# Performance work log

Hardware: AMD Instinct MI355X
Metric: run time of the kernel (lower is better)

Reference implementation:

```python
import jax, jax.numpy as jnp
import numpy as np

N = 500_000          # num nodes
K = 3                # neighbors per star subgraph = graphlet_size - 1
E = N * K            # one subgraph per node -> directed (center, nbr) edges
L = 2                # hop_neighbor
FD = 2               # final_dim = 2**pqc_dim
H = 64               # hidden_dim
NC = 8               # num_classes
NIN = 16             # node_input_dim
EIN = 8              # edge_input_dim


def _lin(k, i, o):
    # torch.nn.Linear-style init scale
    return jax.random.normal(k, (i, o), jnp.float32) * (1.0 / np.sqrt(i))


def setup_inputs() -> dict:
    key = jax.random.key(0)
    ks = jax.random.split(key, 32)
    node_feat = jax.random.normal(ks[0], (N, NIN), jnp.float32)
    edge_attr = jax.random.normal(ks[1], (E, EIN), jnp.float32)
    # edge e = (center, neighbor); centers grouped: edges 3i..3i+2 belong to node i
    centers = jnp.repeat(jnp.arange(N, dtype=jnp.int32), K)
    neighbors = jax.random.randint(ks[2], (E,), 0, N, dtype=jnp.int32)
    edge_index = jnp.stack([centers, neighbors])  # [2, E]
    batch = jnp.zeros((N,), jnp.int32)
    msg_W1 = jnp.stack([_lin(ks[6 + i], 2 * FD, H) for i in range(L)])
    msg_W2 = jnp.stack([_lin(ks[8 + i], H, FD) for i in range(L)])
    upd_W1 = jnp.stack([_lin(ks[10 + i], 2 * FD, H) for i in range(L)])
    upd_W2 = jnp.stack([_lin(ks[12 + i], H, FD) for i in range(L)])
    return dict(
        node_feat=node_feat, edge_attr=edge_attr, edge_index=edge_index, batch=batch,
        Wn=_lin(ks[3], NIN, FD), bn=jnp.zeros((FD,), jnp.float32),
        We=_lin(ks[4], EIN, FD), be=jnp.zeros((FD,), jnp.float32),
        msg_W1=msg_W1, msg_b1=jnp.zeros((L, H), jnp.float32),
        msg_W2=msg_W2, msg_b2=jnp.zeros((L, FD), jnp.float32),
        upd_W1=upd_W1, upd_b1=jnp.zeros((L, H), jnp.float32),
        upd_W2=upd_W2, upd_b2=jnp.zeros((L, FD), jnp.float32),
        fin_W1=_lin(ks[14], FD, H), fin_b1=jnp.zeros((H,), jnp.float32),
        fin_W2=_lin(ks[15], H, NC), fin_b2=jnp.zeros((NC,), jnp.float32),
    )


def _leaky(x):
    return jnp.where(x >= 0, x, 0.1 * x)


def _mlp(x, W1, b1, W2, b2):
    # MLP([din, 64, dout], act=LeakyReLU(0.1)); dropout inactive at eval
    return _leaky(x @ W1 + b1) @ W2 + b2


def reference(node_feat, edge_attr, edge_index, batch, Wn, bn, We, be,
              msg_W1, msg_b1, msg_W2, msg_b2, upd_W1, upd_b1, upd_W2, upd_b2,
              fin_W1, fin_b1, fin_W2, fin_b2):
    ctr = edge_index[0]  # [E] center of each star edge
    nbr = edge_index[1]  # [E] neighbor
    h = node_feat @ Wn + bn      # [N, FD] input_node projection
    e = edge_attr @ We + be      # [E, FD] input_edge projection (fixed across layers)
    for l in range(L):
        # message over each (center, neighbor) edge: concat(edge_feat, nbr_feat)
        msg = _mlp(jnp.concatenate([e, h[nbr]], axis=1),
                   msg_W1[l], msg_b1[l], msg_W2[l], msg_b2[l])  # [E, FD]
        aggr = jax.ops.segment_sum(msg, ctr, num_segments=N)    # [N, FD]
        new = _mlp(jnp.concatenate([h, aggr], axis=1),
                   upd_W1[l], upd_b1[l], upd_W2[l], upd_b2[l])  # [N, FD]
        h = jax.nn.relu(h + new)  # updates_node[center] += new_center; then ReLU
    return _mlp(h, fin_W1, fin_b1, fin_W2, fin_b2)  # [N, NC]
```

## Files before the change

kernel.cpp:

```cpp
#include <hip/hip_runtime.h>

#define NN 500000
#define KK 3
#define EE (NN * KK)
#define HH 64
#define NC 8
#define NIN 16
#define EIN 8

typedef __attribute__((ext_vector_type(2)))  float sf2;
typedef __attribute__((ext_vector_type(4)))  float sf4;
typedef __attribute__((ext_vector_type(8)))  float sf8;
typedef __attribute__((ext_vector_type(16))) float sf16;

__device__ __forceinline__ sf2 sload2(const float* p) {
    sf2 r; asm("s_load_dwordx2 %0, %1, 0x0" : "=s"(r) : "s"(p)); return r;
}
__device__ __forceinline__ sf4 sload4(const float* p) {
    sf4 r; asm("s_load_dwordx4 %0, %1, 0x0" : "=s"(r) : "s"(p)); return r;
}
__device__ __forceinline__ sf8 sload8(const float* p) {
    sf8 r; asm("s_load_dwordx8 %0, %1, 0x0" : "=s"(r) : "s"(p)); return r;
}
__device__ __forceinline__ sf16 sload16(const float* p) {
    sf16 r; asm("s_load_dwordx16 %0, %1, 0x0" : "=s"(r) : "s"(p)); return r;
}

#define SWAIT1(a)           asm volatile("s_waitcnt lgkmcnt(0)" : "+s"(a))
#define SWAIT2(a,b)         asm volatile("s_waitcnt lgkmcnt(0)" : "+s"(a),"+s"(b))
#define SWAIT5(a,b,c,d,e)   asm volatile("s_waitcnt lgkmcnt(0)" : "+s"(a),"+s"(b),"+s"(c),"+s"(d),"+s"(e))
#define SWAIT6(a,b,c,d,e,f) asm volatile("s_waitcnt lgkmcnt(0)" : "+s"(a),"+s"(b),"+s"(c),"+s"(d),"+s"(e),"+s"(f))

__device__ __forceinline__ float leaky(float x) { return fmaxf(x, 0.1f * x); }

__global__ __launch_bounds__(256) void prep_kernel(
    const float* __restrict__ node_feat, const float* __restrict__ edge_attr,
    const float* __restrict__ Wn, const float* __restrict__ bn,
    const float* __restrict__ We, const float* __restrict__ be,
    float* __restrict__ h, float* __restrict__ ep)
{
    sf16 wn0 = sload16(Wn);
    sf16 wn1 = sload16(Wn + 16);
    sf2  bnv = sload2(bn);
    sf16 wev = sload16(We);
    sf2  bev = sload2(be);
    SWAIT5(wn0, wn1, bnv, wev, bev);

    int idx = blockIdx.x * 256 + threadIdx.x;
    if (idx < NN) {
        const float4* x4 = (const float4*)(node_feat + (size_t)idx * NIN);
        float4 v0 = x4[0], v1 = x4[1], v2 = x4[2], v3 = x4[3];
        float xs[16] = {v0.x, v0.y, v0.z, v0.w, v1.x, v1.y, v1.z, v1.w,
                        v2.x, v2.y, v2.z, v2.w, v3.x, v3.y, v3.z, v3.w};
        float a0 = bnv.x, a1 = bnv.y;
#pragma unroll
        for (int i = 0; i < 8; i++) {
            a0 = fmaf(xs[i], wn0[2 * i], a0);
            a1 = fmaf(xs[i], wn0[2 * i + 1], a1);
        }
#pragma unroll
        for (int i = 0; i < 8; i++) {
            a0 = fmaf(xs[8 + i], wn1[2 * i], a0);
            a1 = fmaf(xs[8 + i], wn1[2 * i + 1], a1);
        }
        ((float2*)h)[idx] = make_float2(a0, a1);
    } else if (idx < NN + EE) {
        int eidx = idx - NN;
        const float4* x4 = (const float4*)(edge_attr + (size_t)eidx * EIN);
        float4 v0 = x4[0], v1 = x4[1];
        float xs[8] = {v0.x, v0.y, v0.z, v0.w, v1.x, v1.y, v1.z, v1.w};
        float a0 = bev.x, a1 = bev.y;
#pragma unroll
        for (int i = 0; i < 8; i++) {
            a0 = fmaf(xs[i], wev[2 * i], a0);
            a1 = fmaf(xs[i], wev[2 * i + 1], a1);
        }
        ((float2*)ep)[eidx] = make_float2(a0, a1);
    }
}

template<bool FINAL>
__global__ __launch_bounds__(256) void layer_kernel(
    const float* __restrict__ h_in, const float* __restrict__ e,
    const int* __restrict__ nbr,
    const float* __restrict__ mW1, const float* __restrict__ mb1,
    const float* __restrict__ mW2, const float* __restrict__ mb2,
    const float* __restrict__ uW1, const float* __restrict__ ub1,
    const float* __restrict__ uW2, const float* __restrict__ ub2,
    float* __restrict__ h_out,
    const float* __restrict__ fW1, const float* __restrict__ fb1,
    const float* __restrict__ fW2, const float* __restrict__ fb2,
    float* __restrict__ out)
{
    int i = blockIdx.x * 256 + threadIdx.x;
    if (i >= NN) return;

    sf2 mb2v = sload2(mb2);
    sf2 ub2v = sload2(ub2);
    SWAIT2(mb2v, ub2v);

    float2 hh = ((const float2*)h_in)[i];
    int base = i * KK;
    int n0 = nbr[base + 0], n1 = nbr[base + 1], n2 = nbr[base + 2];
    float2 hn0 = ((const float2*)h_in)[n0];
    float2 hn1 = ((const float2*)h_in)[n1];
    float2 hn2 = ((const float2*)h_in)[n2];
    float2 e0 = ((const float2*)e)[base + 0];
    float2 e1 = ((const float2*)e)[base + 1];
    float2 e2 = ((const float2*)e)[base + 2];

    float a0 = 3.0f * mb2v.x, a1 = 3.0f * mb2v.y;
#pragma unroll 1
    for (int j0 = 0; j0 < HH; j0 += 8) {
        sf8 w0 = sload8(mW1 + j0);
        sf8 w1 = sload8(mW1 + HH + j0);
        sf8 w2 = sload8(mW1 + 2 * HH + j0);
        sf8 w3 = sload8(mW1 + 3 * HH + j0);
        sf8 bb = sload8(mb1 + j0);
        sf16 wc = sload16(mW2 + 2 * j0);
        SWAIT6(w0, w1, w2, w3, bb, wc);
#pragma unroll
        for (int q = 0; q < 8; q++) {
            float t0 = fmaf(e0.x, w0[q], fmaf(e0.y, w1[q], fmaf(hn0.x, w2[q], fmaf(hn0.y, w3[q], bb[q]))));
            float t1 = fmaf(e1.x, w0[q], fmaf(e1.y, w1[q], fmaf(hn1.x, w2[q], fmaf(hn1.y, w3[q], bb[q]))));
            float t2 = fmaf(e2.x, w0[q], fmaf(e2.y, w1[q], fmaf(hn2.x, w2[q], fmaf(hn2.y, w3[q], bb[q]))));
            float ts = leaky(t0) + leaky(t1) + leaky(t2);
            a0 = fmaf(ts, wc[2 * q], a0);
            a1 = fmaf(ts, wc[2 * q + 1], a1);
        }
    }

    float u0 = ub2v.x, u1 = ub2v.y;
#pragma unroll 1
    for (int j0 = 0; j0 < HH; j0 += 8) {
        sf8 w0 = sload8(uW1 + j0);
        sf8 w1 = sload8(uW1 + HH + j0);
        sf8 w2 = sload8(uW1 + 2 * HH + j0);
        sf8 w3 = sload8(uW1 + 3 * HH + j0);
        sf8 bb = sload8(ub1 + j0);
        sf16 wc = sload16(uW2 + 2 * j0);
        SWAIT6(w0, w1, w2, w3, bb, wc);
#pragma unroll
        for (int q = 0; q < 8; q++) {
            float tt = fmaf(hh.x, w0[q], fmaf(hh.y, w1[q], fmaf(a0, w2[q], fmaf(a1, w3[q], bb[q]))));
            tt = leaky(tt);
            u0 = fmaf(tt, wc[2 * q], u0);
            u1 = fmaf(tt, wc[2 * q + 1], u1);
        }
    }
    float nh0 = fmaxf(hh.x + u0, 0.0f);
    float nh1 = fmaxf(hh.y + u1, 0.0f);

    if (!FINAL) {
        ((float2*)h_out)[i] = make_float2(nh0, nh1);
    } else {
        sf8 fb2v = sload8(fb2);
        SWAIT1(fb2v);
        float o[NC];
#pragma unroll
        for (int c = 0; c < NC; c++) o[c] = fb2v[c];
#pragma unroll 1
        for (int j0 = 0; j0 < HH; j0 += 4) {
            sf4 p0 = sload4(fW1 + j0);
            sf4 p1 = sload4(fW1 + HH + j0);
            sf4 pb = sload4(fb1 + j0);
            sf16 q0 = sload16(fW2 + 8 * j0);
            sf16 q1 = sload16(fW2 + 8 * j0 + 16);
            SWAIT5(p0, p1, pb, q0, q1);
#pragma unroll
            for (int qq = 0; qq < 4; qq++) {
                float tt = leaky(fmaf(nh0, p0[qq], fmaf(nh1, p1[qq], pb[qq])));
#pragma unroll
                for (int c = 0; c < NC; c++) {
                    float wv = (qq < 2) ? q0[8 * qq + c] : q1[8 * (qq - 2) + c];
                    o[c] = fmaf(tt, wv, o[c]);
                }
            }
        }
        float4* op = (float4*)(out + (size_t)i * NC);
        op[0] = make_float4(o[0], o[1], o[2], o[3]);
        op[1] = make_float4(o[4], o[5], o[6], o[7]);
    }
}

extern "C" void kernel_launch(void* const* d_in, const int* in_sizes, int n_in,
                              void* d_out, int out_size, void* d_ws, size_t ws_size,
                              hipStream_t stream) {
    const float* node_feat = (const float*)d_in[0];
    const float* edge_attr = (const float*)d_in[1];
    const int* edge_index = (const int*)d_in[2];
    const float* Wn = (const float*)d_in[4];
    const float* bn = (const float*)d_in[5];
    const float* We = (const float*)d_in[6];
    const float* be = (const float*)d_in[7];
    const float* msgW1 = (const float*)d_in[8];
    const float* msgb1 = (const float*)d_in[9];
    const float* msgW2 = (const float*)d_in[10];
    const float* msgb2 = (const float*)d_in[11];
    const float* updW1 = (const float*)d_in[12];
    const float* updb1 = (const float*)d_in[13];
    const float* updW2 = (const float*)d_in[14];
    const float* updb2 = (const float*)d_in[15];
    const float* finW1 = (const float*)d_in[16];
    const float* finb1 = (const float*)d_in[17];
    const float* finW2 = (const float*)d_in[18];
    const float* finb2 = (const float*)d_in[19];
    float* out = (float*)d_out;

    const int* nbr = edge_index + EE;

    char* ws = (char*)d_ws;
    float* hA = (float*)ws;
    float* hB = (float*)(ws + (size_t)NN * 2 * 4);
    float* eP = (float*)(ws + (size_t)NN * 4 * 4);

    const int threads = 256;
    int prep_grid = (NN + EE + threads - 1) / threads;
    prep_kernel<<<prep_grid, threads, 0, stream>>>(node_feat, edge_attr, Wn, bn, We, be, hA, eP);

    int grid = (NN + threads - 1) / threads;
    layer_kernel<false><<<grid, threads, 0, stream>>>(
        hA, eP, nbr,
        msgW1, msgb1, msgW2, msgb2,
        updW1, updb1, updW2, updb2,
        hB, finW1, finb1, finW2, finb2, nullptr);
    layer_kernel<true><<<grid, threads, 0, stream>>>(
        hB, eP, nbr,
        msgW1 + 4 * HH, msgb1 + HH, msgW2 + 2 * HH, msgb2 + 2,
        updW1 + 4 * HH, updb1 + HH, updW2 + 2 * HH, updb2 + 2,
        nullptr, finW1, finb1, finW2, finb2, out);
}
```

Baseline: 213.9 us.

## Compute MLP hidden layers in packed fp16 with pre-packed weights and fdot2

Adds a pack kernel that converts the message, update and final MLP weights into interleaved fp16 pairs. The layer kernels then evaluate the hidden units two at a time with packed fp16 FMA, apply leaky ReLU in packed form, and reduce with fdot2 into fp32 accumulators. Edge projections are stored as duplicated fp16 pairs. The aim is to halve the VALU instruction count of the compute-bound per-node MLPs, at the cost of fp16 rounding error in the hidden activations and one extra small launch.

```diff
diff --git a/kernel.cpp b/kernel.cpp
--- a/kernel.cpp
+++ b/kernel.cpp
@@ -8,36 +8,100 @@
 #define NIN 16
 #define EIN 8
 
+typedef __attribute__((ext_vector_type(2))) _Float16 h2;
 typedef __attribute__((ext_vector_type(2)))  float sf2;
-typedef __attribute__((ext_vector_type(4)))  float sf4;
 typedef __attribute__((ext_vector_type(8)))  float sf8;
 typedef __attribute__((ext_vector_type(16))) float sf16;
 
+using pk_t = decltype(__builtin_amdgcn_cvt_pkrtz(0.f, 0.f));
+
 __device__ __forceinline__ sf2 sload2(const float* p) {
     sf2 r; asm("s_load_dwordx2 %0, %1, 0x0" : "=s"(r) : "s"(p)); return r;
 }
-__device__ __forceinline__ sf4 sload4(const float* p) {
-    sf4 r; asm("s_load_dwordx4 %0, %1, 0x0" : "=s"(r) : "s"(p)); return r;
-}
 __device__ __forceinline__ sf8 sload8(const float* p) {
     sf8 r; asm("s_load_dwordx8 %0, %1, 0x0" : "=s"(r) : "s"(p)); return r;
 }
 __device__ __forceinline__ sf16 sload16(const float* p) {
     sf16 r; asm("s_load_dwordx16 %0, %1, 0x0" : "=s"(r) : "s"(p)); return r;
 }
-
-#define SWAIT1(a)           asm volatile("s_waitcnt lgkmcnt(0)" : "+s"(a))
-#define SWAIT2(a,b)         asm volatile("s_waitcnt lgkmcnt(0)" : "+s"(a),"+s"(b))
-#define SWAIT5(a,b,c,d,e)   asm volatile("s_waitcnt lgkmcnt(0)" : "+s"(a),"+s"(b),"+s"(c),"+s"(d),"+s"(e))
-#define SWAIT6(a,b,c,d,e,f) asm volatile("s_waitcnt lgkmcnt(0)" : "+s"(a),"+s"(b),"+s"(c),"+s"(d),"+s"(e),"+s"(f))
-
-__device__ __forceinline__ float leaky(float x) { return fmaxf(x, 0.1f * x); }
+#define SWAIT1(a)       asm volatile("s_waitcnt lgkmcnt(0)" : "+s"(a))
+#define SWAIT2(a,b)     asm volatile("s_waitcnt lgkmcnt(0)" : "+s"(a),"+s"(b))
+#define SWAIT3(a,b,c)   asm volatile("s_waitcnt lgkmcnt(0)" : "+s"(a),"+s"(b),"+s"(c))
+#define SWAIT5(a,b,c,d,e) asm volatile("s_waitcnt lgkmcnt(0)" : "+s"(a),"+s"(b),"+s"(c),"+s"(d),"+s"(e))
+
+#if __has_builtin(__builtin_elementwise_fma)
+#define PKFMA(a,b,c) __builtin_elementwise_fma((a),(b),(c))
+#else
+#define PKFMA(a,b,c) ((a)*(b)+(c))
+#endif
+
+__device__ __forceinline__ h2 bch2(float f)        { return __builtin_bit_cast(h2, f); }
+__device__ __forceinline__ h2 bch2u(unsigned int u){ return __builtin_bit_cast(h2, u); }
+__device__ __forceinline__ h2 dup16(float f) {
+    return __builtin_bit_cast(h2, __builtin_amdgcn_cvt_pkrtz(f, f));
+}
+__device__ __forceinline__ float fdot2(h2 a, h2 b, float c) {
+#if __has_builtin(__builtin_amdgcn_fdot2)
+    return __builtin_amdgcn_fdot2(__builtin_bit_cast(pk_t, a),
+                                  __builtin_bit_cast(pk_t, b), c, false);
+#else
+    return c + (float)a.x * (float)b.x + (float)a.y * (float)b.y;
+#endif
+}
+__device__ __forceinline__ h2 lk2(h2 x) {
+    h2 c = {(_Float16)0.1f, (_Float16)0.1f};
+    return __builtin_elementwise_max(x, x * c);
+}
+
+__device__ __forceinline__ float pack2(float a, float b) {
+    h2 v; v.x = (_Float16)a; v.y = (_Float16)b;
+    return __builtin_bit_cast(float, v);
+}
+
+__global__ void pack_kernel(
+    const float* __restrict__ msgW1, const float* __restrict__ msgb1, const float* __restrict__ msgW2,
+    const float* __restrict__ updW1, const float* __restrict__ updb1, const float* __restrict__ updW2,
+    const float* __restrict__ finW1, const float* __restrict__ finb1, const float* __restrict__ finW2,
+    float* __restrict__ wpack)
+{
+    int t = threadIdx.x;
+    if (t < 32) {
+        int l = t >> 4, which = (t >> 3) & 1, c = t & 7;
+        const float* W1 = (which ? updW1 : msgW1) + l * 4 * HH;
+        const float* b1 = (which ? updb1 : msgb1) + l * HH;
+        const float* W2 = (which ? updW2 : msgW2) + l * 2 * HH;
+        float* dst = wpack + (l * 2 + which) * 256 + c * 32;
+        int j0 = c * 8;
+        for (int r = 0; r < 4; r++)
+            for (int p = 0; p < 4; p++)
+                dst[r * 4 + p] = pack2(W1[r * HH + j0 + 2 * p], W1[r * HH + j0 + 2 * p + 1]);
+        for (int p = 0; p < 4; p++) {
+            dst[16 + p] = pack2(b1[j0 + 2 * p], b1[j0 + 2 * p + 1]);
+            dst[20 + p] = pack2(W2[(j0 + 2 * p) * 2 + 0], W2[(j0 + 2 * p + 1) * 2 + 0]);
+            dst[24 + p] = pack2(W2[(j0 + 2 * p) * 2 + 1], W2[(j0 + 2 * p + 1) * 2 + 1]);
+            dst[28 + p] = 0.0f;
+        }
+    } else if (t < 40) {
+        int c = t - 32, j0 = c * 8;
+        float* dst = wpack + 1024 + c * 48;
+        for (int p = 0; p < 4; p++) {
+            dst[p]      = pack2(finW1[j0 + 2 * p],      finW1[j0 + 2 * p + 1]);
+            dst[4 + p]  = pack2(finW1[HH + j0 + 2 * p], finW1[HH + j0 + 2 * p + 1]);
+            dst[8 + p]  = pack2(finb1[j0 + 2 * p],      finb1[j0 + 2 * p + 1]);
+            dst[12 + p] = 0.0f;
+        }
+        for (int jp = 0; jp < 4; jp++)
+            for (int cc = 0; cc < NC; cc++)
+                dst[16 + jp * 8 + cc] = pack2(finW2[(j0 + 2 * jp) * NC + cc],
+                                              finW2[(j0 + 2 * jp + 1) * NC + cc]);
+    }
+}
 
 __global__ __launch_bounds__(256) void prep_kernel(
     const float* __restrict__ node_feat, const float* __restrict__ edge_attr,
     const float* __restrict__ Wn, const float* __restrict__ bn,
     const float* __restrict__ We, const float* __restrict__ be,
-    float* __restrict__ h, float* __restrict__ ep)
+    float* __restrict__ h, unsigned int* __restrict__ ep)
 {
     sf16 wn0 = sload16(Wn);
     sf16 wn1 = sload16(Wn + 16);
@@ -75,21 +139,21 @@
             a0 = fmaf(xs[i], wev[2 * i], a0);
             a1 = fmaf(xs[i], wev[2 * i + 1], a1);
         }
-        ((float2*)ep)[eidx] = make_float2(a0, a1);
+        uint2 pe;
+        pe.x = __builtin_bit_cast(unsigned int, dup16(a0));
+        pe.y = __builtin_bit_cast(unsigned int, dup16(a1));
+        ((uint2*)ep)[eidx] = pe;
     }
 }
 
 template<bool FINAL>
 __global__ __launch_bounds__(256) void layer_kernel(
-    const float* __restrict__ h_in, const float* __restrict__ e,
+    const float* __restrict__ h_in, const unsigned int* __restrict__ eP,
     const int* __restrict__ nbr,
-    const float* __restrict__ mW1, const float* __restrict__ mb1,
-    const float* __restrict__ mW2, const float* __restrict__ mb2,
-    const float* __restrict__ uW1, const float* __restrict__ ub1,
-    const float* __restrict__ uW2, const float* __restrict__ ub2,
+    const float* __restrict__ mblk, const float* __restrict__ mb2,
+    const float* __restrict__ ublk, const float* __restrict__ ub2,
     float* __restrict__ h_out,
-    const float* __restrict__ fW1, const float* __restrict__ fb1,
-    const float* __restrict__ fW2, const float* __restrict__ fb2,
+    const float* __restrict__ fblk, const float* __restrict__ fb2,
     float* __restrict__ out)
 {
     int i = blockIdx.x * 256 + threadIdx.x;
@@ -102,50 +166,55 @@
     float2 hh = ((const float2*)h_in)[i];
     int base = i * KK;
     int n0 = nbr[base + 0], n1 = nbr[base + 1], n2 = nbr[base + 2];
-    float2 hn0 = ((const float2*)h_in)[n0];
-    float2 hn1 = ((const float2*)h_in)[n1];
-    float2 hn2 = ((const float2*)h_in)[n2];
-    float2 e0 = ((const float2*)e)[base + 0];
-    float2 e1 = ((const float2*)e)[base + 1];
-    float2 e2 = ((const float2*)e)[base + 2];
+    float2 g0 = ((const float2*)h_in)[n0];
+    float2 g1 = ((const float2*)h_in)[n1];
+    float2 g2 = ((const float2*)h_in)[n2];
+    uint2 pe0 = ((const uint2*)eP)[base + 0];
+    uint2 pe1 = ((const uint2*)eP)[base + 1];
+    uint2 pe2 = ((const uint2*)eP)[base + 2];
+    h2 e0x = bch2u(pe0.x), e0y = bch2u(pe0.y);
+    h2 e1x = bch2u(pe1.x), e1y = bch2u(pe1.y);
+    h2 e2x = bch2u(pe2.x), e2y = bch2u(pe2.y);
+    h2 n0x = dup16(g0.x), n0y = dup16(g0.y);
+    h2 n1x = dup16(g1.x), n1y = dup16(g1.y);
+    h2 n2x = dup16(g2.x), n2y = dup16(g2.y);
 
     float a0 = 3.0f * mb2v.x, a1 = 3.0f * mb2v.y;
 #pragma unroll 1
-    for (int j0 = 0; j0 < HH; j0 += 8) {
-        sf8 w0 = sload8(mW1 + j0);
-        sf8 w1 = sload8(mW1 + HH + j0);
-        sf8 w2 = sload8(mW1 + 2 * HH + j0);
-        sf8 w3 = sload8(mW1 + 3 * HH + j0);
-        sf8 bb = sload8(mb1 + j0);
-        sf16 wc = sload16(mW2 + 2 * j0);
-        SWAIT6(w0, w1, w2, w3, bb, wc);
-#pragma unroll
-        for (int q = 0; q < 8; q++) {
-            float t0 = fmaf(e0.x, w0[q], fmaf(e0.y, w1[q], fmaf(hn0.x, w2[q], fmaf(hn0.y, w3[q], bb[q]))));
-            float t1 = fmaf(e1.x, w0[q], fmaf(e1.y, w1[q], fmaf(hn1.x, w2[q], fmaf(hn1.y, w3[q], bb[q]))));
-            float t2 = fmaf(e2.x, w0[q], fmaf(e2.y, w1[q], fmaf(hn2.x, w2[q], fmaf(hn2.y, w3[q], bb[q]))));
-            float ts = leaky(t0) + leaky(t1) + leaky(t2);
-            a0 = fmaf(ts, wc[2 * q], a0);
-            a1 = fmaf(ts, wc[2 * q + 1], a1);
-        }
-    }
-
+    for (int c = 0; c < 8; c++) {
+        sf16 A = sload16(mblk + c * 32);
+        sf16 B = sload16(mblk + c * 32 + 16);
+        SWAIT2(A, B);
+#pragma unroll
+        for (int jp = 0; jp < 4; jp++) {
+            h2 w0 = bch2(A[jp]), w1 = bch2(A[4 + jp]);
+            h2 w2 = bch2(A[8 + jp]), w3 = bch2(A[12 + jp]);
+            h2 bb = bch2(B[jp]);
+            h2 t0 = PKFMA(e0x, w0, PKFMA(e0y, w1, PKFMA(n0x, w2, PKFMA(n0y, w3, bb))));
+            h2 t1 = PKFMA(e1x, w0, PKFMA(e1y, w1, PKFMA(n1x, w2, PKFMA(n1y, w3, bb))));
+            h2 t2 = PKFMA(e2x, w0, PKFMA(e2y, w1, PKFMA(n2x, w2, PKFMA(n2y, w3, bb))));
+            h2 ts = lk2(t0) + lk2(t1) + lk2(t2);
+            a0 = fdot2(ts, bch2(B[4 + jp]), a0);
+            a1 = fdot2(ts, bch2(B[8 + jp]), a1);
+        }
+    }
+
+    h2 hx = dup16(hh.x), hy = dup16(hh.y), ax = dup16(a0), ay = dup16(a1);
     float u0 = ub2v.x, u1 = ub2v.y;
 #pragma unroll 1
-    for (int j0 = 0; j0 < HH; j0 += 8) {
-        sf8 w0 = sload8(uW1 + j0);
-        sf8 w1 = sload8(uW1 + HH + j0);
-        sf8 w2 = sload8(uW1 + 2 * HH + j0);
-        sf8 w3 = sload8(uW1 + 3 * HH + j0);
-        sf8 bb = sload8(ub1 + j0);
-        sf16 wc = sload16(uW2 + 2 * j0);
-        SWAIT6(w0, w1, w2, w3, bb, wc);
-#pragma unroll
-        for (int q = 0; q < 8; q++) {
-            float tt = fmaf(hh.x, w0[q], fmaf(hh.y, w1[q], fmaf(a0, w2[q], fmaf(a1, w3[q], bb[q]))));
-            tt = leaky(tt);
-            u0 = fmaf(tt, wc[2 * q], u0);
-            u1 = fmaf(tt, wc[2 * q + 1], u1);
+    for (int c = 0; c < 8; c++) {
+        sf16 A = sload16(ublk + c * 32);
+        sf16 B = sload16(ublk + c * 32 + 16);
+        SWAIT2(A, B);
+#pragma unroll
+        for (int jp = 0; jp < 4; jp++) {
+            h2 tt = PKFMA(hx, bch2(A[jp]),
+                    PKFMA(hy, bch2(A[4 + jp]),
+                    PKFMA(ax, bch2(A[8 + jp]),
+                    PKFMA(ay, bch2(A[12 + jp]), bch2(B[jp])))));
+            tt = lk2(tt);
+            u0 = fdot2(tt, bch2(B[4 + jp]), u0);
+            u1 = fdot2(tt, bch2(B[8 + jp]), u1);
         }
     }
     float nh0 = fmaxf(hh.x + u0, 0.0f);
@@ -158,22 +227,21 @@
         SWAIT1(fb2v);
         float o[NC];
 #pragma unroll
-        for (int c = 0; c < NC; c++) o[c] = fb2v[c];
+        for (int cc = 0; cc < NC; cc++) o[cc] = fb2v[cc];
+        h2 nx = dup16(nh0), ny = dup16(nh1);
 #pragma unroll 1
-        for (int j0 = 0; j0 < HH; j0 += 4) {
-            sf4 p0 = sload4(fW1 + j0);
-            sf4 p1 = sload4(fW1 + HH + j0);
-            sf4 pb = sload4(fb1 + j0);
-            sf16 q0 = sload16(fW2 + 8 * j0);
-            sf16 q1 = sload16(fW2 + 8 * j0 + 16);
-            SWAIT5(p0, p1, pb, q0, q1);
-#pragma unroll
-            for (int qq = 0; qq < 4; qq++) {
-                float tt = leaky(fmaf(nh0, p0[qq], fmaf(nh1, p1[qq], pb[qq])));
-#pragma unroll
-                for (int c = 0; c < NC; c++) {
-                    float wv = (qq < 2) ? q0[8 * qq + c] : q1[8 * (qq - 2) + c];
-                    o[c] = fmaf(tt, wv, o[c]);
+        for (int c = 0; c < 8; c++) {
+            sf16 A = sload16(fblk + c * 48);
+            sf16 B = sload16(fblk + c * 48 + 16);
+            sf16 C = sload16(fblk + c * 48 + 32);
+            SWAIT3(A, B, C);
+#pragma unroll
+            for (int jp = 0; jp < 4; jp++) {
+                h2 tt = lk2(PKFMA(nx, bch2(A[jp]), PKFMA(ny, bch2(A[4 + jp]), bch2(A[8 + jp]))));
+#pragma unroll
+                for (int cc = 0; cc < NC; cc++) {
+                    float w = (jp < 2) ? B[(jp & 1) * 8 + cc] : C[(jp & 1) * 8 + cc];
+                    o[cc] = fdot2(tt, bch2(w), o[cc]);
                 }
             }
         }
@@ -212,7 +280,12 @@
     char* ws = (char*)d_ws;
     float* hA = (float*)ws;
     float* hB = (float*)(ws + (size_t)NN * 2 * 4);
-    float* eP = (float*)(ws + (size_t)NN * 4 * 4);
+    unsigned int* eP = (unsigned int*)(ws + (size_t)NN * 4 * 4);
+    float* wpack = (float*)(ws + (size_t)NN * 4 * 4 + (size_t)EE * 2 * 4);
+
+    pack_kernel<<<1, 64, 0, stream>>>(msgW1, msgb1, msgW2,
+                                      updW1, updb1, updW2,
+                                      finW1, finb1, finW2, wpack);
 
     const int threads = 256;
     int prep_grid = (NN + EE + threads - 1) / threads;
@@ -221,12 +294,12 @@
     int grid = (NN + threads - 1) / threads;
     layer_kernel<false><<<grid, threads, 0, stream>>>(
         hA, eP, nbr,
-        msgW1, msgb1, msgW2, msgb2,
-        updW1, updb1, updW2, updb2,
-        hB, finW1, finb1, finW2, finb2, nullptr);
+        wpack + 0 * 256, msgb2,
+        wpack + 1 * 256, updb2,
+        hB, wpack + 1024, finb2, nullptr);
     layer_kernel<true><<<grid, threads, 0, stream>>>(
         hB, eP, nbr,
-        msgW1 + 4 * HH, msgb1 + HH, msgW2 + 2 * HH, msgb2 + 2,
-        updW1 + 4 * HH, updb1 + HH, updW2 + 2 * HH, updb2 + 2,
-        nullptr, finW1, finb1, finW2, finb2, out);
-}
+        wpack + 2 * 256, msgb2 + 2,
+        wpack + 3 * 256, updb2 + 2,
+        nullptr, wpack + 1024, finb2, out);
+}
```

Result: faster. 204.7 us (-4.3%).
